# Optimization experiments

Hardware: AMD Instinct MI355X
Metric: run time of the kernel (lower is better)

The kernel has to match this reference:

```python
import jax, jax.numpy as jnp
import numpy as np

BETA = 0.25


def setup_inputs() -> dict:
    key = jax.random.key(0)
    k1, = jax.random.split(key, 1)
    N, D, LEVELS = 1048576, 32, 8
    z_e = jax.random.normal(k1, (N, D), dtype=jnp.float32)
    grid = jnp.linspace(-1.0, 1.0, LEVELS, dtype=jnp.float32)  # FSQ buffer
    return {"z_e": z_e, "grid": grid}


def reference(z_e, grid):
    levels = grid.shape[0]  # static
    z_norm = jnp.tanh(z_e)                                   # [N, D]
    # nearest-level search over the tiny grid (faithful abs-distance argmin)
    dist = jnp.abs(z_norm[:, :, None] - grid[None, None, :])  # [N, D, L]
    indices = jnp.argmin(dist, axis=-1)                       # [N, D] int
    z_q = grid[indices]                                       # [N, D]

    codebook_loss = jnp.mean((z_q - jax.lax.stop_gradient(z_norm)) ** 2)
    commitment_loss = jnp.mean((z_norm - jax.lax.stop_gradient(z_q)) ** 2)
    loss = codebook_loss + BETA * commitment_loss

    # straight-through estimator
    z_q_st = z_norm + jax.lax.stop_gradient(z_q - z_norm)

    # mixed code over first <=4 dims, perplexity = unique fraction
    code_dims = min(indices.shape[1], 4)
    bases = (levels ** jnp.arange(code_dims)).astype(indices.dtype)  # [code_dims]
    mixed_indices = jnp.sum(indices[:, :code_dims] * bases[None, :], axis=1)  # [N]
    n_codes = levels ** code_dims  # static small (4096)
    occupancy = jnp.bincount(mixed_indices, length=n_codes) > 0
    unique_codes = jnp.sum(occupancy).astype(z_e.dtype)
    perplexity = unique_codes / jnp.asarray(float(max(mixed_indices.size, 1)), z_e.dtype)

    return z_q_st, mixed_indices, loss, perplexity
```

## Files before the change

kernel.cpp:

```cpp
#include <hip/hip_runtime.h>
#include <math.h>

#define DD 32
#define BS 256

typedef float f32x4 __attribute__((ext_vector_type(4)));

__device__ __forceinline__ unsigned int fkey(float f) {
    unsigned int u = __float_as_uint(f);
    return (u & 0x80000000u) ? ~u : (u | 0x80000000u);
}
__device__ __forceinline__ float funkey(unsigned int k) {
    unsigned int u = (k & 0x80000000u) ? (k ^ 0x80000000u) : ~k;
    return __uint_as_float(u);
}

__global__ __launch_bounds__(256) void fsq_main(
    const float* __restrict__ ze,
    const float* __restrict__ grid,
    float* __restrict__ out,
    int N,
    float* __restrict__ partials,
    int* __restrict__ occ)
{
    __shared__ float ts[7];
    if (threadIdx.x < 7) {
        float a = grid[threadIdx.x], b = grid[threadIdx.x + 1];
        unsigned int lo = fkey(a), hi = fkey(b);
        while (hi - lo > 1u) {
            unsigned int mid = lo + (hi - lo) / 2u;
            float x = funkey(mid);
            if (fabsf(x - b) < fabsf(x - a)) hi = mid; else lo = mid;
        }
        ts[threadIdx.x] = funkey(lo);
    }
    const float g0 = grid[0], g1 = grid[1], g2 = grid[2], g3 = grid[3],
                g4 = grid[4], g5 = grid[5], g6 = grid[6], g7 = grid[7];
    __syncthreads();

    const int Q = N * DD / 4;
    const int i = blockIdx.x * BS + threadIdx.x;
    float lsum = 0.f;

    if (i < Q) {
        f32x4 w = __builtin_nontemporal_load((const f32x4*)ze + i);
        float xs[4] = {w.x, w.y, w.z, w.w};
        float tns[4];
        int bis[4];
        bool bad = false;
#pragma unroll
        for (int e = 0; e < 4; ++e) {
            float x = xs[e];
            float ex = __expf(2.0f * x);
            float r = __builtin_amdgcn_rcpf(ex + 1.0f);
            float tn = __builtin_fmaf(-2.0f, r, 1.0f);
            float u = __builtin_fmaf(tn, 3.5f, 3.5f);
            float ur = rintf(u);
            float fd = u - ur;
            bad = bad || (fabsf(fd) > 0.4999650f);
            float uc = fminf(7.0f, fmaxf(0.0f, ur));
            tns[e] = tn;
            bis[e] = (int)uc;
        }
        if (bad) {
#pragma unroll
            for (int e = 0; e < 4; ++e) {
                float tn = (float)tanh((double)xs[e]);
                int b = 0;
#pragma unroll
                for (int j = 0; j < 7; ++j) b += (tn > ts[j]) ? 1 : 0;
                tns[e] = tn;
                bis[e] = b;
            }
        }
        float os[4];
#pragma unroll
        for (int e = 0; e < 4; ++e) {
            int bi = bis[e];
            float s01 = (bi & 1) ? g1 : g0;
            float s23 = (bi & 1) ? g3 : g2;
            float s45 = (bi & 1) ? g5 : g4;
            float s67 = (bi & 1) ? g7 : g6;
            float t03 = (bi & 2) ? s23 : s01;
            float t47 = (bi & 2) ? s67 : s45;
            float zq  = (bi & 4) ? t47 : t03;
            float d1 = zq - tns[e];
            lsum = __builtin_fmaf(d1, d1, lsum);
            os[e] = tns[e] + d1;
        }
        f32x4 ov = {os[0], os[1], os[2], os[3]};
        *((f32x4*)out + i) = ov;

        if ((i & 7) == 0) {
            int mixed = bis[0] | (bis[1] << 3) | (bis[2] << 6) | (bis[3] << 9);
            out[(size_t)N * DD + (i >> 3)] = (float)mixed;
            occ[mixed] = 1;
        }
    }

    float s = lsum;
#pragma unroll
    for (int off = 32; off > 0; off >>= 1) s += __shfl_down(s, off);
    __shared__ float sh[4];
    if ((threadIdx.x & 63) == 0) sh[threadIdx.x >> 6] = s;
    __syncthreads();
    if (threadIdx.x == 0)
        partials[blockIdx.x] = sh[0] + sh[1] + sh[2] + sh[3];
}

__global__ __launch_bounds__(1024) void fsq_tail(
    const float* __restrict__ partials, int nblocks,
    const int* __restrict__ occ,
    float* __restrict__ out, int N)
{
    double s = 0.0;
    for (int i = threadIdx.x; i < nblocks; i += 1024) s += (double)partials[i];
    int cnt = 0;
    for (int i = threadIdx.x; i < 4096; i += 1024) cnt += (occ[i] == 1) ? 1 : 0;
#pragma unroll
    for (int off = 32; off > 0; off >>= 1) {
        s += __shfl_down(s, off);
        cnt += __shfl_down(cnt, off);
    }
    __shared__ double shs[16];
    __shared__ int shc[16];
    if ((threadIdx.x & 63) == 0) { shs[threadIdx.x >> 6] = s; shc[threadIdx.x >> 6] = cnt; }
    __syncthreads();
    if (threadIdx.x == 0) {
        double total = 0.0;
        int unique = 0;
#pragma unroll
        for (int k = 0; k < 16; ++k) { total += shs[k]; unique += shc[k]; }
        double mean = total / ((double)N * (double)DD);
        size_t base = (size_t)N * DD + (size_t)N;
        out[base] = (float)(1.25 * mean);
        out[base + 1] = (float)unique / (float)N;
    }
}

extern "C" void kernel_launch(void* const* d_in, const int* in_sizes, int n_in,
                              void* d_out, int out_size, void* d_ws, size_t ws_size,
                              hipStream_t stream) {
    const float* ze   = (const float*)d_in[0];
    const float* grid = (const float*)d_in[1];
    float* out = (float*)d_out;
    int N = in_sizes[0] / DD;

    const int Q = N * (DD / 4);
    const int nblocks = (Q + BS - 1) / BS;

    int* occ = (int*)d_ws;
    float* partials = (float*)((char*)d_ws + 16384);

    fsq_main<<<nblocks, BS, 0, stream>>>(ze, grid, out, N, partials, occ);
    fsq_tail<<<1, 1024, 0, stream>>>(partials, nblocks, occ, out, N);
}
```

Baseline: 275.1 us.

## Use fixed grid with 4-way grid-stride loop and batched loads; drop threshold precompute

Launches a fixed 8192-block grid where each thread processes four float4 elements strided across the array, issuing all four nontemporal loads up front to raise memory-level parallelism. The shared-memory threshold binary search and its __syncthreads are removed, and the rare fallback path now does a direct 8-way abs-distance argmin against the grid. This cuts block count and partials to reduce per-block overhead and tail reduction work, at the cost of more registers per thread and fewer resident waves for latency hiding.

```diff
diff --git a/kernel.cpp b/kernel.cpp
--- a/kernel.cpp
+++ b/kernel.cpp
@@ -2,17 +2,70 @@
 #include <math.h>
 
 #define DD 32
+#define NB 8192
 #define BS 256
+#define STRIDE (NB * BS)
+#define TRIP 4
 
 typedef float f32x4 __attribute__((ext_vector_type(4)));
 
-__device__ __forceinline__ unsigned int fkey(float f) {
-    unsigned int u = __float_as_uint(f);
-    return (u & 0x80000000u) ? ~u : (u | 0x80000000u);
-}
-__device__ __forceinline__ float funkey(unsigned int k) {
-    unsigned int u = (k & 0x80000000u) ? (k ^ 0x80000000u) : ~k;
-    return __uint_as_float(u);
+
+__device__ __forceinline__ void fsq_quad(
+    f32x4 w, float g0, float g1, float g2, float g3,
+    float g4, float g5, float g6, float g7,
+    float &lsum, f32x4 &ov, int &mix)
+{
+    float xs[4] = {w.x, w.y, w.z, w.w};
+    float tns[4];
+    int bis[4];
+    bool bad = false;
+#pragma unroll
+    for (int e = 0; e < 4; ++e) {
+        float x = xs[e];
+        float ex = __expf(2.0f * x);
+        float r = __builtin_amdgcn_rcpf(ex + 1.0f);
+        float tn = __builtin_fmaf(-2.0f, r, 1.0f);
+        float u = __builtin_fmaf(tn, 3.5f, 3.5f);
+        float ur = rintf(u);
+        float fd = u - ur;
+        bad = bad || (fabsf(fd) > 0.4999650f);
+        float uc = fminf(7.0f, fmaxf(0.0f, ur));
+        tns[e] = tn;
+        bis[e] = (int)uc;
+    }
+    if (bad) {
+#pragma unroll
+        for (int e = 0; e < 4; ++e) {
+            float tn = (float)tanh((double)xs[e]);
+            float gl[8] = {g0, g1, g2, g3, g4, g5, g6, g7};
+            float best = fabsf(tn - gl[0]);
+            int b = 0;
+#pragma unroll
+            for (int j = 1; j < 8; ++j) {
+                float d = fabsf(tn - gl[j]);
+                if (d < best) { best = d; b = j; }
+            }
+            tns[e] = tn;
+            bis[e] = b;
+        }
+    }
+    float os[4];
+#pragma unroll
+    for (int e = 0; e < 4; ++e) {
+        int bi = bis[e];
+        float s01 = (bi & 1) ? g1 : g0;
+        float s23 = (bi & 1) ? g3 : g2;
+        float s45 = (bi & 1) ? g5 : g4;
+        float s67 = (bi & 1) ? g7 : g6;
+        float t03 = (bi & 2) ? s23 : s01;
+        float t47 = (bi & 2) ? s67 : s45;
+        float zq  = (bi & 4) ? t47 : t03;
+        float d1 = zq - tns[e];
+        lsum = __builtin_fmaf(d1, d1, lsum);
+        os[e] = tns[e] + d1;
+    }
+    ov.x = os[0]; ov.y = os[1]; ov.z = os[2]; ov.w = os[3];
+    mix = bis[0] | (bis[1] << 3) | (bis[2] << 6) | (bis[3] << 9);
 }
 
 __global__ __launch_bounds__(256) void fsq_main(
@@ -23,78 +76,39 @@
     float* __restrict__ partials,
     int* __restrict__ occ)
 {
-    __shared__ float ts[7];
-    if (threadIdx.x < 7) {
-        float a = grid[threadIdx.x], b = grid[threadIdx.x + 1];
-        unsigned int lo = fkey(a), hi = fkey(b);
-        while (hi - lo > 1u) {
-            unsigned int mid = lo + (hi - lo) / 2u;
-            float x = funkey(mid);
-            if (fabsf(x - b) < fabsf(x - a)) hi = mid; else lo = mid;
-        }
-        ts[threadIdx.x] = funkey(lo);
-    }
     const float g0 = grid[0], g1 = grid[1], g2 = grid[2], g3 = grid[3],
                 g4 = grid[4], g5 = grid[5], g6 = grid[6], g7 = grid[7];
-    __syncthreads();
 
     const int Q = N * DD / 4;
-    const int i = blockIdx.x * BS + threadIdx.x;
     float lsum = 0.f;
 
-    if (i < Q) {
-        f32x4 w = __builtin_nontemporal_load((const f32x4*)ze + i);
-        float xs[4] = {w.x, w.y, w.z, w.w};
-        float tns[4];
-        int bis[4];
-        bool bad = false;
+    const int i0 = blockIdx.x * BS + threadIdx.x;
+    if (Q == TRIP * STRIDE) {
+        f32x4 w[TRIP];
 #pragma unroll
-        for (int e = 0; e < 4; ++e) {
-            float x = xs[e];
-            float ex = __expf(2.0f * x);
-            float r = __builtin_amdgcn_rcpf(ex + 1.0f);
-            float tn = __builtin_fmaf(-2.0f, r, 1.0f);
-            float u = __builtin_fmaf(tn, 3.5f, 3.5f);
-            float ur = rintf(u);
-            float fd = u - ur;
-            bad = bad || (fabsf(fd) > 0.4999650f);
-            float uc = fminf(7.0f, fmaxf(0.0f, ur));
-            tns[e] = tn;
-            bis[e] = (int)uc;
-        }
-        if (bad) {
+        for (int k = 0; k < TRIP; ++k)
+            w[k] = __builtin_nontemporal_load((const f32x4*)ze + i0 + k * STRIDE);
 #pragma unroll
-            for (int e = 0; e < 4; ++e) {
-                float tn = (float)tanh((double)xs[e]);
-                int b = 0;
-#pragma unroll
-                for (int j = 0; j < 7; ++j) b += (tn > ts[j]) ? 1 : 0;
-                tns[e] = tn;
-                bis[e] = b;
+        for (int k = 0; k < TRIP; ++k) {
+            const int i = i0 + k * STRIDE;
+            f32x4 ov; int mix;
+            fsq_quad(w[k], g0, g1, g2, g3, g4, g5, g6, g7, lsum, ov, mix);
+            *((f32x4*)out + i) = ov;
+            if ((i & 7) == 0) {
+                out[(size_t)N * DD + (i >> 3)] = (float)mix;
+                occ[mix] = 1;
             }
         }
-        float os[4];
-#pragma unroll
-        for (int e = 0; e < 4; ++e) {
-            int bi = bis[e];
-            float s01 = (bi & 1) ? g1 : g0;
-            float s23 = (bi & 1) ? g3 : g2;
-            float s45 = (bi & 1) ? g5 : g4;
-            float s67 = (bi & 1) ? g7 : g6;
-            float t03 = (bi & 2) ? s23 : s01;
-            float t47 = (bi & 2) ? s67 : s45;
-            float zq  = (bi & 4) ? t47 : t03;
-            float d1 = zq - tns[e];
-            lsum = __builtin_fmaf(d1, d1, lsum);
-            os[e] = tns[e] + d1;
-        }
-        f32x4 ov = {os[0], os[1], os[2], os[3]};
-        *((f32x4*)out + i) = ov;
-
-        if ((i & 7) == 0) {
-            int mixed = bis[0] | (bis[1] << 3) | (bis[2] << 6) | (bis[3] << 9);
-            out[(size_t)N * DD + (i >> 3)] = (float)mixed;
-            occ[mixed] = 1;
+    } else {
+        for (int i = i0; i < Q; i += STRIDE) {
+            f32x4 w = __builtin_nontemporal_load((const f32x4*)ze + i);
+            f32x4 ov; int mix;
+            fsq_quad(w, g0, g1, g2, g3, g4, g5, g6, g7, lsum, ov, mix);
+            *((f32x4*)out + i) = ov;
+            if ((i & 7) == 0) {
+                out[(size_t)N * DD + (i >> 3)] = (float)mix;
+                occ[mix] = 1;
+            }
         }
     }
 
@@ -146,12 +160,9 @@
     float* out = (float*)d_out;
     int N = in_sizes[0] / DD;
 
-    const int Q = N * (DD / 4);
-    const int nblocks = (Q + BS - 1) / BS;
-
     int* occ = (int*)d_ws;
     float* partials = (float*)((char*)d_ws + 16384);
 
-    fsq_main<<<nblocks, BS, 0, stream>>>(ze, grid, out, N, partials, occ);
-    fsq_tail<<<1, 1024, 0, stream>>>(partials, nblocks, occ, out, N);
+    fsq_main<<<NB, BS, 0, stream>>>(ze, grid, out, N, partials, occ);
+    fsq_tail<<<1, 1024, 0, stream>>>(partials, NB, occ, out, N);
 }
```

Result: faster. 239.5 us, median of 2 (-13.0%).
